# Optimization experiments

Hardware: AMD Instinct MI355X
Metric: run time of the kernel (lower is better)

## Reference

```python
import jax, jax.numpy as jnp
import numpy as np

EPS = 1e-06


def setup_inputs() -> dict:
    key = jax.random.key(0)
    k1, k2, k3 = jax.random.split(key, 3)
    B, L, S, C = 128, 512, 512, 64
    q = jax.random.normal(k1, (B, L, C), dtype=jnp.float32)
    k = jax.random.normal(k2, (B, S, C), dtype=jnp.float32)
    labels = jax.random.randint(k3, (B, L, S), 0, 2, dtype=jnp.int64)
    return {"q": q, "k": k, "labels": labels}


def reference(q, k, labels):
    # sim: [B, L, S], mapped to (0, 1) via (1 + cos-like sim) / 2
    sim = (1.0 + jnp.einsum('blc,bsc->bls', q, k)) * 0.5

    # column-wise stats (over L) -> [B, S]; torch.std uses ddof=1 (unbiased)
    col = (jnp.max(sim, axis=1) - jnp.mean(sim, axis=1)) / jnp.std(sim, axis=1, ddof=1)
    sharp1 = jax.nn.softmax(col, axis=-1)  # [B, S]

    # row-wise stats (over S) -> [B, L]
    row = (jnp.max(sim, axis=2) - jnp.mean(sim, axis=2)) / jnp.std(sim, axis=2, ddof=1)
    sharp2 = jax.nn.softmax(row, axis=-1)  # [B, L]

    simc = jnp.clip(sim, EPS, 1.0 - EPS)
    nll = -jnp.log(simc)                    # [B, L, S]
    nll_neg = -jnp.log(1.0 - simc)          # [B, L, S]

    pos = (labels == 1).astype(sim.dtype)
    neg = (labels == 0).astype(sim.dtype)

    # masked sums per sample, weighted by sharpness (broadcast over rows/cols)
    loss1 = jnp.sum(nll * sharp1[:, None, :] * pos, axis=(1, 2))  # [B]
    loss2 = jnp.sum(nll * sharp2[:, :, None] * pos, axis=(1, 2))  # [B]
    loss3 = jnp.sum(nll_neg * neg, axis=(1, 2)) / jnp.sum(neg, axis=(1, 2))  # [B]

    losses = (loss1 + loss2) * 0.5 + loss3
    return (sharp1, jnp.mean(losses))
```

## Files before the change

kernel.cpp:

```cpp
#include <hip/hip_runtime.h>

#define EPSF 1e-6f
#define LN2F 0.69314718055994531f

typedef _Float16 half8 __attribute__((ext_vector_type(8)));
typedef float f32x4 __attribute__((ext_vector_type(4)));

constexpr int B = 128, L = 512, S = 512, C = 64;
constexpr int TILE_R = 64;
constexpr int TILES  = L / TILE_R;
constexpr int CHUNK  = 64;
constexpr int NCHUNK = S / CHUNK;
constexpr int HALVES = 2;
constexpr int CPB    = NCHUNK / HALVES;

constexpr size_t WS_COLMAX = 0;
constexpr size_t WS_COLSUM = WS_COLMAX + (size_t)B * TILES * S;
constexpr size_t WS_COLSSQ = WS_COLSUM + (size_t)B * TILES * S;
constexpr size_t WS_COLP1  = WS_COLSSQ + (size_t)B * TILES * S;
constexpr size_t WS_ROWMAX = WS_COLP1  + (size_t)B * TILES * S;
constexpr size_t WS_ROWSUM = WS_ROWMAX + (size_t)B * L * HALVES;
constexpr size_t WS_ROWSSQ = WS_ROWSUM + (size_t)B * L * HALVES;
constexpr size_t WS_ROWP2  = WS_ROWSSQ + (size_t)B * L * HALVES;
constexpr size_t WS_NEGS   = WS_ROWP2  + (size_t)B * L * HALVES;
constexpr size_t WS_NEGC   = WS_NEGS   + (size_t)B * TILES * HALVES;

__device__ inline void loadTile(const float* __restrict__ g, float4 v[4], int t)
{
    const float* src = g + (t >> 2) * 64 + (t & 3) * 16;
    v[0] = *(const float4*)(src);
    v[1] = *(const float4*)(src + 4);
    v[2] = *(const float4*)(src + 8);
    v[3] = *(const float4*)(src + 12);
}

__device__ inline void stageW(const float4 v4[4], half8 (*hiA)[64], half8 (*loA)[64], int t)
{
    const int row = t >> 2, c0 = (t & 3) * 16;
    const float v[16] = {v4[0].x, v4[0].y, v4[0].z, v4[0].w, v4[1].x, v4[1].y, v4[1].z, v4[1].w,
                         v4[2].x, v4[2].y, v4[2].z, v4[2].w, v4[3].x, v4[3].y, v4[3].z, v4[3].w};
#pragma unroll
    for (int o = 0; o < 2; ++o) {
        const int cb     = c0 + o * 8;
        const int idx    = (row >> 4) * 2 + (cb >> 5);
        const int lane_s = (((cb >> 3) & 3) << 4) + (row & 15);
        half8 h, l;
#pragma unroll
        for (int j = 0; j < 8; ++j) {
            float f = v[o * 8 + j];
            _Float16 hi = (_Float16)f;
            h[j] = hi;
            l[j] = (_Float16)(f - (float)hi);
        }
        hiA[idx][lane_s] = h;
        loA[idx][lane_s] = l;
    }
}

__global__ __launch_bounds__(256) __attribute__((amdgpu_waves_per_eu(3, 8)))
void pass1_kernel(const float* __restrict__ q, const float* __restrict__ kmat,
                  const int* __restrict__ labels, float* __restrict__ ws,
                  float* __restrict__ outp)
{
    __shared__ half8 khiF[8][64], kloF[8][64];
    __shared__ float4 colred4[4][CHUNK];
    __shared__ float nred[4][2];

    const int bidx = blockIdx.x;
    const int b    = bidx / (TILES * HALVES);
    const int rem  = bidx % (TILES * HALVES);
    const int tile = rem >> 1;
    const int half = rem & 1;
    const int chbase = half * CPB;
    const int tid  = threadIdx.x;
    const int lane = tid & 63;
    const int wave = tid >> 6;
    const int l15  = lane & 15;
    const int quad = lane >> 4;
    const int rowbase = tile * TILE_R;

    if (bidx == 0 && tid == 0) outp[(size_t)B * S] = 0.f;

    float* colmax_p = ws + WS_COLMAX;
    float* colsum_p = ws + WS_COLSUM;
    float* colssq_p = ws + WS_COLSSQ;
    float* colp1_p  = ws + WS_COLP1;
    float* rowmax_p = ws + WS_ROWMAX;
    float* rowsum_p = ws + WS_ROWSUM;
    float* rowssq_p = ws + WS_ROWSSQ;
    float* rowp2_p  = ws + WS_ROWP2;
    float* negs_p   = ws + WS_NEGS;
    float* negc_p   = ws + WS_NEGC;

    const float* kb = kmat + (size_t)b * S * C;
    const int*   lb = labels + ((size_t)b * L + rowbase) * S;

    float4 tv[4];
    loadTile(q + ((size_t)b * L + rowbase) * C, tv, tid);
    stageW(tv, khiF, kloF, tid);
    int labn[16];
#pragma unroll
    for (int ct = 0; ct < 4; ++ct)
#pragma unroll
        for (int r = 0; r < 4; ++r)
            labn[ct * 4 + r] = __builtin_nontemporal_load(
                &lb[(size_t)(wave * 16 + quad * 4 + r) * S
                    + chbase * CHUNK + ct * 16 + l15]);
    __syncthreads();
    half8 ah0 = khiF[wave * 2 + 0][lane], ah1 = khiF[wave * 2 + 1][lane];
    half8 al0 = kloF[wave * 2 + 0][lane], al1 = kloF[wave * 2 + 1][lane];
    loadTile(kb + (size_t)chbase * CHUNK * C, tv, tid);

    float rmax[4], rsum[4], rssq[4], rp2[4];
#pragma unroll
    for (int i = 0; i < 4; ++i) { rmax[i] = -3.4e38f; rsum[i] = 0.f; rssq[i] = 0.f; rp2[i] = 0.f; }
    float nlsum = 0.f;
    int   possum = 0;

    for (int c4 = 0; c4 < CPB; ++c4) {
        const int ch = chbase + c4;
        __syncthreads();
        if (c4 > 0 && tid < CHUNK) {
            float4 v = colred4[0][tid];
            float m0 = v.x, s1 = v.y, s2 = v.z, pp = v.w;
#pragma unroll
            for (int w = 1; w < 4; ++w) {
                float4 u = colred4[w][tid];
                m0 = fmaxf(m0, u.x); s1 += u.y; s2 += u.z; pp += u.w;
            }
            size_t idx = ((size_t)b * TILES + tile) * S + (ch - 1) * CHUNK + tid;
            colmax_p[idx] = m0; colsum_p[idx] = s1; colssq_p[idx] = s2; colp1_p[idx] = pp;
        }
        stageW(tv, khiF, kloF, tid);
        if (c4 + 1 < CPB)
            loadTile(kb + (size_t)(ch + 1) * CHUNK * C, tv, tid);
        __syncthreads();

        f32x4 acc[4];
#pragma unroll
        for (int ct = 0; ct < 4; ++ct) {
            half8 bh0 = khiF[ct * 2 + 0][lane], bh1 = khiF[ct * 2 + 1][lane];
            half8 bl0 = kloF[ct * 2 + 0][lane], bl1 = kloF[ct * 2 + 1][lane];
            f32x4 a = {0.f, 0.f, 0.f, 0.f};
            a = __builtin_amdgcn_mfma_f32_16x16x32_f16(ah0, bh0, a, 0, 0, 0);
            a = __builtin_amdgcn_mfma_f32_16x16x32_f16(ah0, bl0, a, 0, 0, 0);
            a = __builtin_amdgcn_mfma_f32_16x16x32_f16(al0, bh0, a, 0, 0, 0);
            a = __builtin_amdgcn_mfma_f32_16x16x32_f16(ah1, bh1, a, 0, 0, 0);
            a = __builtin_amdgcn_mfma_f32_16x16x32_f16(ah1, bl1, a, 0, 0, 0);
            a = __builtin_amdgcn_mfma_f32_16x16x32_f16(al1, bh1, a, 0, 0, 0);
            acc[ct] = a;
        }

#pragma unroll
        for (int ct = 0; ct < 4; ++ct) {
            float cmax = -3.4e38f, csum = 0.f, cssq = 0.f, cp1 = 0.f;
#pragma unroll
            for (int r = 0; r < 4; ++r) {
                int lab = labn[ct * 4 + r];
                float sim = fmaf(0.5f, acc[ct][r], 0.5f);
                rmax[r] = fmaxf(rmax[r], sim);
                rsum[r] += sim;
                rssq[r] = fmaf(sim, sim, rssq[r]);
                cmax = fmaxf(cmax, sim);
                csum += sim;
                cssq = fmaf(sim, sim, cssq);
                bool  isp = (lab == 1);
                float tt  = isp ? sim : (1.f - sim);
                tt = fminf(fmaxf(tt, EPSF), 1.f - EPSF);
                float l2 = __log2f(tt);
                float pv = isp ? l2 : 0.f;
                rp2[r] += pv;
                cp1   += pv;
                nlsum += l2;
                possum += lab;
            }
            cp1 *= -LN2F;
#pragma unroll
            for (int m = 16; m <= 32; m <<= 1) {
                cmax = fmaxf(cmax, __shfl_xor(cmax, m, 64));
                csum += __shfl_xor(csum, m, 64);
                cssq += __shfl_xor(cssq, m, 64);
                cp1  += __shfl_xor(cp1,  m, 64);
            }
            if (lane < 16)
                colred4[wave][ct * 16 + l15] = make_float4(cmax, csum, cssq, cp1);
        }

        if (c4 + 1 < CPB) {
#pragma unroll
            for (int ct = 0; ct < 4; ++ct)
#pragma unroll
                for (int r = 0; r < 4; ++r)
                    labn[ct * 4 + r] = __builtin_nontemporal_load(
                        &lb[(size_t)(wave * 16 + quad * 4 + r) * S
                            + (ch + 1) * CHUNK + ct * 16 + l15]);
        }
    }

    __syncthreads();
    if (tid < CHUNK) {
        float4 v = colred4[0][tid];
        float m0 = v.x, s1 = v.y, s2 = v.z, pp = v.w;
#pragma unroll
        for (int w = 1; w < 4; ++w) {
            float4 u = colred4[w][tid];
            m0 = fmaxf(m0, u.x); s1 += u.y; s2 += u.z; pp += u.w;
        }
        size_t idx = ((size_t)b * TILES + tile) * S + (chbase + CPB - 1) * CHUNK + tid;
        colmax_p[idx] = m0; colsum_p[idx] = s1; colssq_p[idx] = s2; colp1_p[idx] = pp;
    }

#pragma unroll
    for (int r = 0; r < 4; ++r) rp2[r] *= -LN2F;
    float negsum = fmaf(-LN2F, nlsum, -(rp2[0] + rp2[1] + rp2[2] + rp2[3]));

#pragma unroll
    for (int r = 0; r < 4; ++r) {
#pragma unroll
        for (int m = 1; m <= 8; m <<= 1) {
            rmax[r] = fmaxf(rmax[r], __shfl_xor(rmax[r], m, 64));
            rsum[r] += __shfl_xor(rsum[r], m, 64);
            rssq[r] += __shfl_xor(rssq[r], m, 64);
            rp2[r]  += __shfl_xor(rp2[r],  m, 64);
        }
    }
    if (l15 == 0) {
#pragma unroll
        for (int r = 0; r < 4; ++r) {
            size_t idx = ((size_t)b * L + rowbase + wave * 16 + quad * 4 + r) * HALVES + half;
            rowmax_p[idx] = rmax[r]; rowsum_p[idx] = rsum[r];
            rowssq_p[idx] = rssq[r]; rowp2_p[idx]  = rp2[r];
        }
    }

    float negcnt = (float)(16 * CPB - possum);
#pragma unroll
    for (int m = 1; m <= 32; m <<= 1) {
        negsum += __shfl_xor(negsum, m, 64);
        negcnt += __shfl_xor(negcnt, m, 64);
    }
    if (lane == 0) { nred[wave][0] = negsum; nred[wave][1] = negcnt; }
    __syncthreads();
    if (tid == 0) {
        float ns = 0.f, nc = 0.f;
        for (int w = 0; w < 4; ++w) { ns += nred[w][0]; nc += nred[w][1]; }
        negs_p[bidx] = ns; negc_p[bidx] = nc;
    }
}

template <bool MAX>
__device__ inline float bred(float v, float* red)
{
#pragma unroll
    for (int m = 1; m <= 32; m <<= 1) {
        float o = __shfl_xor(v, m, 64);
        v = MAX ? fmaxf(v, o) : (v + o);
    }
    const int wave = threadIdx.x >> 6;
    const int lane = threadIdx.x & 63;
    if (lane == 0) red[wave] = v;
    __syncthreads();
    if (threadIdx.x == 0) {
        float r = red[0];
        for (int w = 1; w < 8; ++w) r = MAX ? fmaxf(r, red[w]) : (r + red[w]);
        red[8] = r;
    }
    __syncthreads();
    float out = red[8];
    __syncthreads();
    return out;
}

__global__ __launch_bounds__(512)
void pass2_kernel(const float* __restrict__ ws, float* __restrict__ out)
{
    __shared__ float red[9];
    const int b = blockIdx.x;
    const int s = threadIdx.x;

    if (blockIdx.y == 0) {
        const float* colmax_p = ws + WS_COLMAX;
        const float* colsum_p = ws + WS_COLSUM;
        const float* colssq_p = ws + WS_COLSSQ;
        const float* colp1_p  = ws + WS_COLP1;

        float m = -3.4e38f, sm = 0.f, sq = 0.f, p1 = 0.f;
#pragma unroll
        for (int t = 0; t < TILES; ++t) {
            size_t idx = ((size_t)b * TILES + t) * S + s;
            m = fmaxf(m, colmax_p[idx]);
            sm += colsum_p[idx];
            sq += colssq_p[idx];
            p1 += colp1_p[idx];
        }
        float mean  = sm * (1.f / L);
        float var   = (sq - sm * sm * (1.f / L)) * (1.f / (L - 1));
        float score = (m - mean) / sqrtf(var);

        float gmax = bred<true>(score, red);
        float e    = __expf(score - gmax);
        float esum = bred<false>(e, red);
        float sharp1 = e / esum;
        out[(size_t)b * S + s] = sharp1;
        float loss1 = bred<false>(sharp1 * p1, red);
        if (s == 0) atomicAdd(out + (size_t)B * S, loss1 * (0.5f / B));
    } else {
        const float* rowmax_p = ws + WS_ROWMAX;
        const float* rowsum_p = ws + WS_ROWSUM;
        const float* rowssq_p = ws + WS_ROWSSQ;
        const float* rowp2_p  = ws + WS_ROWP2;
        const float* negs_p   = ws + WS_NEGS;
        const float* negc_p   = ws + WS_NEGC;

        size_t ridx = ((size_t)b * L + s) * HALVES;
        float m2 = rowmax_p[ridx], sm2 = rowsum_p[ridx];
        float sq2 = rowssq_p[ridx], p2 = rowp2_p[ridx];
#pragma unroll
        for (int h = 1; h < HALVES; ++h) {
            m2 = fmaxf(m2, rowmax_p[ridx + h]);
            sm2 += rowsum_p[ridx + h];
            sq2 += rowssq_p[ridx + h];
            p2  += rowp2_p[ridx + h];
        }
        float mean2  = sm2 * (1.f / S);
        float var2   = (sq2 - sm2 * sm2 * (1.f / S)) * (1.f / (S - 1));
        float score2 = (m2 - mean2) / sqrtf(var2);

        float gmax2 = bred<true>(score2, red);
        float e2    = __expf(score2 - gmax2);
        float esum2 = bred<false>(e2, red);
        float loss2 = bred<false>((e2 / esum2) * p2, red);

        if (s == 0) {
            float ns = 0.f, nc = 0.f;
            for (int t = 0; t < TILES * HALVES; ++t) {
                ns += negs_p[b * TILES * HALVES + t];
                nc += negc_p[b * TILES * HALVES + t];
            }
            atomicAdd(out + (size_t)B * S, (0.5f * loss2 + ns / nc) * (1.f / B));
        }
    }
}

extern "C" void kernel_launch(void* const* d_in, const int* in_sizes, int n_in,
                              void* d_out, int out_size, void* d_ws, size_t ws_size,
                              hipStream_t stream)
{
    const float* q      = (const float*)d_in[0];
    const float* k      = (const float*)d_in[1];
    const int*   labels = (const int*)d_in[2];
    float* out = (float*)d_out;
    float* ws  = (float*)d_ws;

    pass1_kernel<<<dim3(B * TILES * HALVES), dim3(256), 0, stream>>>(q, k, labels, ws, out);
    pass2_kernel<<<dim3(B, 2), dim3(512), 0, stream>>>(ws, out);
}
```

Measured before the change: 236.5 us.

## Fuse pass2 finalization into pass1 via last-block-done atomic counters

```diff
diff --git a/kernel.cpp b/kernel.cpp
--- a/kernel.cpp
+++ b/kernel.cpp
@@ -13,6 +13,7 @@
 constexpr int NCHUNK = S / CHUNK;
 constexpr int HALVES = 2;
 constexpr int CPB    = NCHUNK / HALVES;
+constexpr int BPB    = TILES * HALVES;
 
 constexpr size_t WS_COLMAX = 0;
 constexpr size_t WS_COLSUM = WS_COLMAX + (size_t)B * TILES * S;
@@ -24,6 +25,7 @@
 constexpr size_t WS_ROWP2  = WS_ROWSSQ + (size_t)B * L * HALVES;
 constexpr size_t WS_NEGS   = WS_ROWP2  + (size_t)B * L * HALVES;
 constexpr size_t WS_NEGC   = WS_NEGS   + (size_t)B * TILES * HALVES;
+constexpr size_t WS_CNT    = WS_NEGC   + (size_t)B * TILES * HALVES;
 
 __device__ inline void loadTile(const float* __restrict__ g, float4 v[4], int t)
 {
@@ -57,6 +59,28 @@
     }
 }
 
+template <bool MAX>
+__device__ inline float bred4(float v, float* red)
+{
+#pragma unroll
+    for (int m = 1; m <= 32; m <<= 1) {
+        float o = __shfl_xor(v, m, 64);
+        v = MAX ? fmaxf(v, o) : (v + o);
+    }
+    const int wave = threadIdx.x >> 6;
+    if ((threadIdx.x & 63) == 0) red[wave] = v;
+    __syncthreads();
+    if (threadIdx.x == 0) {
+        float r = red[0];
+        for (int w = 1; w < 4; ++w) r = MAX ? fmaxf(r, red[w]) : (r + red[w]);
+        red[4] = r;
+    }
+    __syncthreads();
+    float out = red[4];
+    __syncthreads();
+    return out;
+}
+
 __global__ __launch_bounds__(256) __attribute__((amdgpu_waves_per_eu(3, 8)))
 void pass1_kernel(const float* __restrict__ q, const float* __restrict__ kmat,
                   const int* __restrict__ labels, float* __restrict__ ws,
@@ -65,10 +89,12 @@
     __shared__ half8 khiF[8][64], kloF[8][64];
     __shared__ float4 colred4[4][CHUNK];
     __shared__ float nred[4][2];
+    __shared__ float fred[5];
+    __shared__ int   finflag;
 
     const int bidx = blockIdx.x;
-    const int b    = bidx / (TILES * HALVES);
-    const int rem  = bidx % (TILES * HALVES);
+    const int b    = bidx / BPB;
+    const int rem  = bidx % BPB;
     const int tile = rem >> 1;
     const int half = rem & 1;
     const int chbase = half * CPB;
@@ -78,8 +104,6 @@
     const int l15  = lane & 15;
     const int quad = lane >> 4;
     const int rowbase = tile * TILE_R;
-
-    if (bidx == 0 && tid == 0) outp[(size_t)B * S] = 0.f;
 
     float* colmax_p = ws + WS_COLMAX;
     float* colsum_p = ws + WS_COLSUM;
@@ -91,6 +115,8 @@
     float* rowp2_p  = ws + WS_ROWP2;
     float* negs_p   = ws + WS_NEGS;
     float* negc_p   = ws + WS_NEGC;
+    int*   cnt_p    = (int*)(ws + WS_CNT);
+    float* acc_p    = ws + WS_CNT + 129;
 
     const float* kb = kmat + (size_t)b * S * C;
     const int*   lb = labels + ((size_t)b * L + rowbase) * S;
@@ -246,99 +272,75 @@
         for (int w = 0; w < 4; ++w) { ns += nred[w][0]; nc += nred[w][1]; }
         negs_p[bidx] = ns; negc_p[bidx] = nc;
     }
-}
-
-template <bool MAX>
-__device__ inline float bred(float v, float* red)
-{
-#pragma unroll
-    for (int m = 1; m <= 32; m <<= 1) {
-        float o = __shfl_xor(v, m, 64);
-        v = MAX ? fmaxf(v, o) : (v + o);
-    }
-    const int wave = threadIdx.x >> 6;
-    const int lane = threadIdx.x & 63;
-    if (lane == 0) red[wave] = v;
-    __syncthreads();
-    if (threadIdx.x == 0) {
-        float r = red[0];
-        for (int w = 1; w < 8; ++w) r = MAX ? fmaxf(r, red[w]) : (r + red[w]);
-        red[8] = r;
-    }
-    __syncthreads();
-    float out = red[8];
-    __syncthreads();
-    return out;
-}
-
-__global__ __launch_bounds__(512)
-void pass2_kernel(const float* __restrict__ ws, float* __restrict__ out)
-{
-    __shared__ float red[9];
-    const int b = blockIdx.x;
-    const int s = threadIdx.x;
-
-    if (blockIdx.y == 0) {
-        const float* colmax_p = ws + WS_COLMAX;
-        const float* colsum_p = ws + WS_COLSUM;
-        const float* colssq_p = ws + WS_COLSSQ;
-        const float* colp1_p  = ws + WS_COLP1;
-
-        float m = -3.4e38f, sm = 0.f, sq = 0.f, p1 = 0.f;
+
+    __syncthreads();
+    __threadfence();
+    if (tid == 0) {
+        int old = atomicAdd(&cnt_p[b], 1);
+        finflag = (old == BPB - 1);
+    }
+    __syncthreads();
+    if (!finflag) return;
+    __threadfence();
+
+    float score[2], p1v[2];
+#pragma unroll
+    for (int j = 0; j < 2; ++j) {
+        const int s = tid + j * 256;
+        float m = -3.4e38f, sm = 0.f, sq = 0.f, pp = 0.f;
 #pragma unroll
         for (int t = 0; t < TILES; ++t) {
             size_t idx = ((size_t)b * TILES + t) * S + s;
             m = fmaxf(m, colmax_p[idx]);
             sm += colsum_p[idx];
             sq += colssq_p[idx];
-            p1 += colp1_p[idx];
-        }
-        float mean  = sm * (1.f / L);
-        float var   = (sq - sm * sm * (1.f / L)) * (1.f / (L - 1));
-        float score = (m - mean) / sqrtf(var);
-
-        float gmax = bred<true>(score, red);
-        float e    = __expf(score - gmax);
-        float esum = bred<false>(e, red);
-        float sharp1 = e / esum;
-        out[(size_t)b * S + s] = sharp1;
-        float loss1 = bred<false>(sharp1 * p1, red);
-        if (s == 0) atomicAdd(out + (size_t)B * S, loss1 * (0.5f / B));
-    } else {
-        const float* rowmax_p = ws + WS_ROWMAX;
-        const float* rowsum_p = ws + WS_ROWSUM;
-        const float* rowssq_p = ws + WS_ROWSSQ;
-        const float* rowp2_p  = ws + WS_ROWP2;
-        const float* negs_p   = ws + WS_NEGS;
-        const float* negc_p   = ws + WS_NEGC;
-
-        size_t ridx = ((size_t)b * L + s) * HALVES;
-        float m2 = rowmax_p[ridx], sm2 = rowsum_p[ridx];
-        float sq2 = rowssq_p[ridx], p2 = rowp2_p[ridx];
-#pragma unroll
-        for (int h = 1; h < HALVES; ++h) {
-            m2 = fmaxf(m2, rowmax_p[ridx + h]);
-            sm2 += rowsum_p[ridx + h];
-            sq2 += rowssq_p[ridx + h];
-            p2  += rowp2_p[ridx + h];
-        }
-        float mean2  = sm2 * (1.f / S);
-        float var2   = (sq2 - sm2 * sm2 * (1.f / S)) * (1.f / (S - 1));
-        float score2 = (m2 - mean2) / sqrtf(var2);
-
-        float gmax2 = bred<true>(score2, red);
-        float e2    = __expf(score2 - gmax2);
-        float esum2 = bred<false>(e2, red);
-        float loss2 = bred<false>((e2 / esum2) * p2, red);
-
-        if (s == 0) {
-            float ns = 0.f, nc = 0.f;
-            for (int t = 0; t < TILES * HALVES; ++t) {
-                ns += negs_p[b * TILES * HALVES + t];
-                nc += negc_p[b * TILES * HALVES + t];
-            }
-            atomicAdd(out + (size_t)B * S, (0.5f * loss2 + ns / nc) * (1.f / B));
-        }
+            pp += colp1_p[idx];
+        }
+        float mean = sm * (1.f / L);
+        float var  = (sq - sm * sm * (1.f / L)) * (1.f / (L - 1));
+        score[j] = (m - mean) / sqrtf(var);
+        p1v[j]   = pp;
+    }
+    float gmax = bred4<true>(fmaxf(score[0], score[1]), fred);
+    float e0 = __expf(score[0] - gmax), e1 = __expf(score[1] - gmax);
+    float esum = bred4<false>(e0 + e1, fred);
+    float inv = 1.f / esum;
+    outp[(size_t)b * S + tid]       = e0 * inv;
+    outp[(size_t)b * S + tid + 256] = e1 * inv;
+    float loss1 = bred4<false>(e0 * inv * p1v[0] + e1 * inv * p1v[1], fred);
+
+    float score2[2], p2v[2];
+#pragma unroll
+    for (int j = 0; j < 2; ++j) {
+        const int row = tid + j * 256;
+        size_t ridx = ((size_t)b * L + row) * HALVES;
+        float m2  = fmaxf(rowmax_p[ridx], rowmax_p[ridx + 1]);
+        float sm2 = rowsum_p[ridx] + rowsum_p[ridx + 1];
+        float sq2 = rowssq_p[ridx] + rowssq_p[ridx + 1];
+        float p2  = rowp2_p[ridx]  + rowp2_p[ridx + 1];
+        float mean2 = sm2 * (1.f / S);
+        float var2  = (sq2 - sm2 * sm2 * (1.f / S)) * (1.f / (S - 1));
+        score2[j] = (m2 - mean2) / sqrtf(var2);
+        p2v[j]    = p2;
+    }
+    float gmax2 = bred4<true>(fmaxf(score2[0], score2[1]), fred);
+    float f0 = __expf(score2[0] - gmax2), f1 = __expf(score2[1] - gmax2);
+    float esum2 = bred4<false>(f0 + f1, fred);
+    float inv2 = 1.f / esum2;
+    float loss2 = bred4<false>(f0 * inv2 * p2v[0] + f1 * inv2 * p2v[1], fred);
+
+    if (tid == 0) {
+        float ns = 0.f, nc = 0.f;
+        for (int t = 0; t < BPB; ++t) {
+            ns += negs_p[b * BPB + t];
+            nc += negc_p[b * BPB + t];
+        }
+        float lb_total = (0.5f * (loss1 + loss2) + ns / nc) * (1.f / B);
+        atomicAdd(acc_p, lb_total);
+        __threadfence();
+        int old2 = atomicAdd(&cnt_p[B], 1);
+        if (old2 == B - 1)
+            outp[(size_t)B * S] = atomicAdd(acc_p, 0.f);
     }
 }
 
@@ -352,6 +354,7 @@
     float* out = (float*)d_out;
     float* ws  = (float*)d_ws;
 
+    hipMemsetAsync(ws + WS_CNT, 0, 130 * sizeof(float), stream);
+
     pass1_kernel<<<dim3(B * TILES * HALVES), dim3(256), 0, stream>>>(q, k, labels, ws, out);
-    pass2_kernel<<<dim3(B, 2), dim3(512), 0, stream>>>(ws, out);
-}
+}
```

After: 667.8 us. 2.82x slower.
